# Kernel optimization log

Hardware: AMD Instinct MI355X
Metric: run time of the kernel (lower is better)

The kernel has to match this reference:

```python
import jax, jax.numpy as jnp
import numpy as np

NEG_INF = -1e30  # stands in for -inf on the H-diagonal (matches softmax zeroing)


def conv1x1(x, W, b):
    # x: [B,C,H,W], W: [O,C], b: [O] -> [B,O,H,W]
    return jnp.einsum('bchw,oc->bohw', x, W) + b[None, :, None, None]


def setup_inputs() -> dict:
    key = jax.random.key(0)
    ks = jax.random.split(key, 8)
    B, C, H, W = 4, 64, 256, 256
    C8 = C // 8
    s = 1.0 / np.sqrt(C)
    return {
        'x': jax.random.normal(ks[0], (B, C, H, W), jnp.float32),
        'Wq': jax.random.normal(ks[1], (C8, C), jnp.float32) * s,
        'bq': jnp.zeros((C8,), jnp.float32),
        'Wk': jax.random.normal(ks[2], (C8, C), jnp.float32) * s,
        'bk': jnp.zeros((C8,), jnp.float32),
        'Wv': jax.random.normal(ks[3], (C, C), jnp.float32) * s,
        'bv': jnp.zeros((C,), jnp.float32),
        'gamma': jnp.zeros((1,), jnp.float32),
    }


def reference(x, Wq, bq, Wk, bk, Wv, bv, gamma):
    B, C, H, W = x.shape
    q = conv1x1(x, Wq, bq)   # [B,C8,H,W]
    k = conv1x1(x, Wk, bk)   # [B,C8,H,W]
    v = conv1x1(x, Wv, bv)   # [B,C,H,W]

    # Row (height-axis) attention energies with -inf on the self (diagonal) entry.
    energy_H = jnp.einsum('bchw,bcjw->bhwj', q, k)               # [B,H,W,H]
    diag = jnp.eye(H, dtype=bool)[:, None, :]                    # [H,1,H]
    energy_H = jnp.where(diag[None], NEG_INF, energy_H)
    # Column (width-axis) attention energies.
    energy_W = jnp.einsum('bchw,bchj->bhwj', q, k)               # [B,H,W,W]

    att = jax.nn.softmax(jnp.concatenate([energy_H, energy_W], axis=3), axis=3)
    att_H, att_W = att[..., :H], att[..., H:]                    # [B,H,W,H], [B,H,W,W]

    out_H = jnp.einsum('bcjw,bhwj->bchw', v, att_H)
    out_W = jnp.einsum('bchj,bhwj->bchw', v, att_W)
    return gamma[0] * (out_H + out_W) + x
```

## Files before the change

kernel.cpp:

```cpp
#include <hip/hip_runtime.h>

#define Bn 4
#define Cn 64
#define Hn 256
#define Wn 256
#define HWn 65536

typedef unsigned int u32;
typedef __attribute__((ext_vector_type(2))) unsigned int u32x2;
typedef __attribute__((ext_vector_type(8))) short bf16x8;
typedef __attribute__((ext_vector_type(4))) float f32x4;
typedef __attribute__((ext_vector_type(16))) float f32x16;

__device__ __forceinline__ unsigned short f2b(float f) {
    union { float f; unsigned u; } v; v.f = f;
    return (unsigned short)(v.u >> 16);
}
__device__ __forceinline__ float b2f(unsigned short s) {
    union { float f; unsigned u; } v; v.u = ((unsigned)s) << 16;
    return v.f;
}
__device__ __forceinline__ u32 cvtpk(float lo, float hi) {
    u32 r;
    asm("v_cvt_pk_bf16_f32 %0, %1, %2" : "=v"(r) : "v"(lo), "v"(hi));
    return r;
}
__device__ __forceinline__ void vswap(u32& a, u32& b) {
    asm volatile("v_permlane32_swap_b32 %0, %1" : "+v"(a), "+v"(b));
}
__device__ __forceinline__ float pair_other(float v, int lane) {
    union { float f; u32 u; } A; A.f = v;
    u32 a = A.u, b = A.u;
    vswap(a, b);
    union { u32 u; float f; } R; R.u = (lane < 32) ? b : a;
    return R.f;
}
__device__ __forceinline__ bf16x8 expPack(const f32x16& e, int base, float& ss) {
    float p0 = __expf(e[base + 0]), p1 = __expf(e[base + 1]);
    u32 A = cvtpk(p0, p1); ss += p0 + p1;
    float p4 = __expf(e[base + 4]), p5 = __expf(e[base + 5]);
    u32 B = cvtpk(p4, p5); ss += p4 + p5;
    vswap(A, B);
    float p2 = __expf(e[base + 2]), p3 = __expf(e[base + 3]);
    u32 C = cvtpk(p2, p3); ss += p2 + p3;
    float p6 = __expf(e[base + 6]), p7 = __expf(e[base + 7]);
    u32 D = cvtpk(p6, p7); ss += p6 + p7;
    vswap(C, D);
    union { u32 w[4]; bf16x8 v; } u;
    u.w[0] = A; u.w[1] = C; u.w[2] = B; u.w[3] = D;
    return u.v;
}

__global__ __launch_bounds__(256) void k_proj(
    const float* __restrict__ x,
    const float* __restrict__ Wq, const float* __restrict__ bq,
    const float* __restrict__ Wk, const float* __restrict__ bk,
    const float* __restrict__ Wv, const float* __restrict__ bv,
    unsigned short* __restrict__ qbr, unsigned short* __restrict__ kbr,
    unsigned short* __restrict__ v_row)
{
    __shared__ __align__(16) char Xl[2][16384];
    int t = threadIdx.x, lane = t & 63, wv = t >> 6;
    int row16 = lane & 15, g = lane >> 4;
    int u0 = blockIdx.x * 4;

    bf16x8 Af[5][2];
    #pragma unroll
    for (int m = 0; m < 5; ++m) {
        const float* wrow;
        if (m == 0) wrow = (row16 < 8) ? (Wq + row16 * 64) : (Wk + (row16 - 8) * 64);
        else        wrow = Wv + (size_t)((m - 1) * 16 + row16) * 64;
        #pragma unroll
        for (int ks = 0; ks < 2; ++ks) {
            int c0 = ks * 32 + g * 8;
            f32x4 w0 = *(const f32x4*)(wrow + c0);
            f32x4 w1 = *(const f32x4*)(wrow + c0 + 4);
            bf16x8 a;
            a[0] = (short)f2b(w0[0]); a[1] = (short)f2b(w0[1]);
            a[2] = (short)f2b(w0[2]); a[3] = (short)f2b(w0[3]);
            a[4] = (short)f2b(w1[0]); a[5] = (short)f2b(w1[1]);
            a[6] = (short)f2b(w1[2]); a[7] = (short)f2b(w1[3]);
            Af[m][ks] = a;
        }
    }

    int px4 = (t & 31) * 4;
    int cbase = (t >> 5) << 2;

    f32x4 st[2][8];
    {
        int u = u0;
        int b = u >> 9, rest = u & 511, h = rest >> 1, half = rest & 1;
        const float* xb2 = x + (size_t)b * Cn * HWn + (size_t)h * Wn + half * 128;
        #pragma unroll
        for (int pass = 0; pass < 2; ++pass) {
            int c0s = cbase + pass * 32;
            #pragma unroll
            for (int j = 0; j < 4; ++j)
                st[0][pass * 4 + j] = *(const f32x4*)(xb2 + (size_t)(c0s + j) * HWn + px4);
        }
    }

    #pragma unroll
    for (int ui = 0; ui < 4; ++ui) {
        int u = u0 + ui;
        int b = u >> 9, rest = u & 511, h = rest >> 1, half = rest & 1;
        int cur = ui & 1;

        #pragma unroll
        for (int pass = 0; pass < 2; ++pass) {
            int c0s = cbase + pass * 32;
            #pragma unroll
            for (int i = 0; i < 4; ++i) {
                int px = px4 + i;
                u32x2 w;
                w[0] = (u32)f2b(st[cur][pass * 4 + 0][i]) | ((u32)f2b(st[cur][pass * 4 + 1][i]) << 16);
                w[1] = (u32)f2b(st[cur][pass * 4 + 2][i]) | ((u32)f2b(st[cur][pass * 4 + 3][i]) << 16);
                unsigned addr = (unsigned)(px * 128)
                              + (((unsigned)(c0s * 2)) ^ ((((unsigned)px >> 3) & 7) << 4));
                *(u32x2*)(Xl[cur] + addr) = w;
            }
        }
        __syncthreads();

        if (ui < 3) {
            int un = u + 1;
            int bn = un >> 9, restn = un & 511, hn = restn >> 1, halfn = restn & 1;
            const float* xb2 = x + (size_t)bn * Cn * HWn + (size_t)hn * Wn + halfn * 128;
            #pragma unroll
            for (int pass = 0; pass < 2; ++pass) {
                int c0s = cbase + pass * 32;
                #pragma unroll
                for (int j = 0; j < 4; ++j)
                    st[cur ^ 1][pass * 4 + j] = *(const f32x4*)(xb2 + (size_t)(c0s + j) * HWn + px4);
            }
        }

        f32x4 acc[5][2];
        #pragma unroll
        for (int m = 0; m < 5; ++m)
            #pragma unroll
            for (int nt = 0; nt < 2; ++nt)
                acc[m][nt] = (f32x4){0.f, 0.f, 0.f, 0.f};

        #pragma unroll
        for (int nt = 0; nt < 2; ++nt) {
            int px = wv * 32 + nt * 16 + row16;
            #pragma unroll
            for (int ks = 0; ks < 2; ++ks) {
                int c0 = ks * 32 + g * 8;
                unsigned addr = (unsigned)(px * 128)
                              + (((unsigned)(c0 * 2)) ^ ((((unsigned)px >> 3) & 7) << 4));
                bf16x8 bf = *(const bf16x8*)(Xl[cur] + addr);
                #pragma unroll
                for (int m = 0; m < 5; ++m)
                    acc[m][nt] = __builtin_amdgcn_mfma_f32_16x16x32_bf16(Af[m][ks], bf, acc[m][nt], 0, 0, 0);
            }
        }

        f32x4 bQK = (g < 2) ? *(const f32x4*)(bq + g * 4)
                            : *(const f32x4*)(bk + (g - 2) * 4);
        #pragma unroll
        for (int nt = 0; nt < 2; ++nt) {
            int p = half * 128 + wv * 32 + nt * 16 + row16;
            f32x4 d = acc[0][nt];
            d[0] += bQK[0]; d[1] += bQK[1]; d[2] += bQK[2]; d[3] += bQK[3];
            u32 w0 = (u32)f2b(d[0]) | ((u32)f2b(d[1]) << 16);
            u32 w1 = (u32)f2b(d[2]) | ((u32)f2b(d[3]) << 16);
            size_t roff = ((size_t)(b * Hn + h) * Wn + p) * 8 + (size_t)((g & 1) * 4);
            if (g < 2) {
                *(u32*)(qbr + roff) = w0; *(u32*)(qbr + roff + 2) = w1;
            } else {
                *(u32*)(kbr + roff) = w0; *(u32*)(kbr + roff + 2) = w1;
            }
            #pragma unroll
            for (int m = 1; m < 5; ++m) {
                f32x4 bV = *(const f32x4*)(bv + (m - 1) * 16 + g * 4);
                unsigned short* vp = v_row + (size_t)b * Cn * HWn
                                   + (size_t)((m - 1) * 16 + g * 4) * HWn
                                   + (size_t)h * Wn + p;
                #pragma unroll
                for (int r = 0; r < 4; ++r)
                    vp[(size_t)r * HWn] = f2b(acc[m][nt][r] + bV[r]);
            }
        }
    }
}

__global__ __launch_bounds__(256) void k_tr_bf16(
    const unsigned short* __restrict__ in, unsigned short* __restrict__ out,
    int R, int Ccols)
{
    __shared__ unsigned short tile[64][66];
    int t = threadIdx.x;
    int lr = t >> 6, lc = t & 63;
    int tilesC = Ccols >> 6;
    int per_b = (R >> 6) * tilesC;
    int bid = blockIdx.x;
    int b = bid / per_b;
    int rem = bid - b * per_b;
    int r0 = (rem / tilesC) << 6;
    int c0 = (rem - (rem / tilesC) * tilesC) << 6;
    const unsigned short* ip = in + (size_t)b * R * Ccols;
    unsigned short* op = out + (size_t)b * R * Ccols;
    #pragma unroll
    for (int i = 0; i < 16; ++i) {
        int r = lr * 16 + i;
        tile[r][lc] = ip[(size_t)(r0 + r) * Ccols + c0 + lc];
    }
    __syncthreads();
    #pragma unroll
    for (int i = 0; i < 16; ++i) {
        int c = lr * 16 + i;
        op[(size_t)(c0 + c) * R + r0 + lc] = tile[lc][c];
    }
}

__global__ __launch_bounds__(256, 2) void k_attnH(
    const unsigned short* __restrict__ qbr, const unsigned short* __restrict__ kbr,
    const unsigned short* __restrict__ vT,
    unsigned short* __restrict__ ohT,
    float* __restrict__ sH)
{
    __shared__ __align__(16) unsigned short Vl[16384];
    int t = threadIdx.x, lane = t & 63, wv = t >> 6;
    int l31 = lane & 31, hi = lane >> 5;
    int bid = blockIdx.x;
    int qh = bid & 1;
    int rest = bid >> 1, b = rest >> 8, w = rest & 255;

    const char* vsrc = (const char*)(vT + ((size_t)(b * Wn + w)) * Cn * Hn);
    #pragma unroll
    for (int p = 0; p < 8; ++p) {
        int lin = p * 4096 + t * 16;
        int c = lin >> 9;
        f32x4 d = *(const f32x4*)(vsrc + lin);
        unsigned dst = (unsigned)lin ^ ((unsigned)(c & 7) << 4);
        *(f32x4*)((char*)Vl + dst) = d;
    }

    bf16x8 zer = {};
    int qtA = qh * 4 + wv;
    int q = qtA * 32 + l31;
    bf16x8 Qf, Kf[8];
    {
        bf16x8 v = *(const bf16x8*)(qbr + ((size_t)(b * Hn + q) * Wn + w) * 8);
        Qf = (hi == 0) ? v : zer;
    }
    #pragma unroll
    for (int jt = 0; jt < 8; ++jt) {
        int j = jt * 32 + l31;
        bf16x8 v = *(const bf16x8*)(kbr + ((size_t)(b * Hn + j) * Wn + w) * 8);
        Kf[jt] = (hi == 0) ? v : zer;
    }
    __syncthreads();

    f32x16 Oa = {}, Ob = {};
    float s = 0.f;
    #pragma unroll
    for (int jt = 0; jt < 8; ++jt) {
        f32x16 zc = {};
        f32x16 e = __builtin_amdgcn_mfma_f32_32x32x16_bf16(Kf[jt], Qf, zc, 0, 0, 0);
        if (jt == qtA) {
            #pragma unroll
            for (int r = 0; r < 16; ++r) {
                int rl = (r & 3) + 8 * (r >> 2) + 4 * hi;
                e[r] = (rl == l31) ? -1e30f : e[r];
            }
        }
        bf16x8 P0 = expPack(e, 0, s);
        bf16x8 P1 = expPack(e, 8, s);
        #pragma unroll
        for (int k2 = 0; k2 < 2; ++k2) {
            int ktA = jt * 2 + k2;
            bf16x8 Pf = k2 ? P1 : P0;
            #pragma unroll
            for (int ct = 0; ct < 2; ++ct) {
                int c = ct * 32 + l31;
                unsigned ad = ((unsigned)(c * 512 + ktA * 32 + hi * 16))
                            ^ ((unsigned)(c & 7) << 4);
                bf16x8 Vf = *(const bf16x8*)((const char*)Vl + ad);
                if (ct == 0) Oa = __builtin_amdgcn_mfma_f32_32x32x16_bf16(Vf, Pf, Oa, 0, 0, 0);
                else         Ob = __builtin_amdgcn_mfma_f32_32x32x16_bf16(Vf, Pf, Ob, 0, 0, 0);
            }
        }
    }
    float s_tot = s + pair_other(s, lane);
    if (hi == 0) {
        size_t so = ((size_t)(b * Wn + w)) * Hn + q;
        sH[so] = s_tot;
    }
    unsigned short* ob = ohT + ((size_t)(b * Wn + w)) * Cn * Hn;
    #pragma unroll
    for (int ct = 0; ct < 2; ++ct) {
        #pragma unroll
        for (int r = 0; r < 16; ++r) {
            int c = (r & 3) + 8 * (r >> 2) + 4 * hi + ct * 32;
            float val = ct ? Ob[r] : Oa[r];
            ob[(size_t)c * Hn + q] = f2b(val);
        }
    }
}

__global__ __launch_bounds__(256, 2) void k_attnW(
    const unsigned short* __restrict__ qbr, const unsigned short* __restrict__ kbr,
    const unsigned short* __restrict__ v_row,
    const unsigned short* __restrict__ oh_row,
    const float* __restrict__ sH,
    const float* __restrict__ x, const float* __restrict__ gamma,
    float* __restrict__ out)
{
    __shared__ __align__(16) unsigned short Vl[16384];
    int t = threadIdx.x, lane = t & 63, wv = t >> 6;
    int l31 = lane & 31, hi = lane >> 5;
    int bid = blockIdx.x;
    int qh = bid & 1;
    int rest = bid >> 1, b = rest >> 8, h = rest & 255;

    #pragma unroll
    for (int p = 0; p < 8; ++p) {
        int lin = p * 4096 + t * 16;
        int c = lin >> 9, off = lin & 511;
        const char* src = (const char*)(v_row + ((size_t)(b * Cn + c)) * HWn + (size_t)h * Wn) + off;
        f32x4 d = *(const f32x4*)src;
        unsigned dst = (unsigned)lin ^ ((unsigned)(c & 7) << 4);
        *(f32x4*)((char*)Vl + dst) = d;
    }

    const unsigned short* qb = qbr + ((size_t)(b * Hn + h)) * Wn * 8;
    const unsigned short* kb = kbr + ((size_t)(b * Hn + h)) * Wn * 8;
    bf16x8 zer = {};
    int q = qh * 128 + wv * 32 + l31;
    bf16x8 Qf, Kf[8];
    {
        bf16x8 v = *(const bf16x8*)(qb + (size_t)q * 8);
        Qf = (hi == 0) ? v : zer;
    }
    #pragma unroll
    for (int jt = 0; jt < 8; ++jt) {
        int j = jt * 32 + l31;
        bf16x8 v = *(const bf16x8*)(kb + (size_t)j * 8);
        Kf[jt] = (hi == 0) ? v : zer;
    }
    float g = gamma[0];
    __syncthreads();

    f32x16 Oa = {}, Ob = {};
    float s = 0.f;
    #pragma unroll
    for (int jt = 0; jt < 8; ++jt) {
        f32x16 zc = {};
        f32x16 e = __builtin_amdgcn_mfma_f32_32x32x16_bf16(Kf[jt], Qf, zc, 0, 0, 0);
        bf16x8 P0 = expPack(e, 0, s);
        bf16x8 P1 = expPack(e, 8, s);
        #pragma unroll
        for (int k2 = 0; k2 < 2; ++k2) {
            int ktA = jt * 2 + k2;
            bf16x8 Pf = k2 ? P1 : P0;
            #pragma unroll
            for (int ct = 0; ct < 2; ++ct) {
                int c = ct * 32 + l31;
                unsigned ad = ((unsigned)(c * 512 + ktA * 32 + hi * 16))
                            ^ ((unsigned)(c & 7) << 4);
                bf16x8 Vf = *(const bf16x8*)((const char*)Vl + ad);
                if (ct == 0) Oa = __builtin_amdgcn_mfma_f32_32x32x16_bf16(Vf, Pf, Oa, 0, 0, 0);
                else         Ob = __builtin_amdgcn_mfma_f32_32x32x16_bf16(Vf, Pf, Ob, 0, 0, 0);
            }
        }
    }
    float s_tot = s + pair_other(s, lane);
    size_t so = ((size_t)(b * Wn + q)) * Hn + h;
    float sh = sH[so];
    float gi = g / (s_tot + sh);
    #pragma unroll
    for (int ct = 0; ct < 2; ++ct) {
        #pragma unroll
        for (int r = 0; r < 16; ++r) {
            int c = (r & 3) + 8 * (r >> 2) + 4 * hi + ct * 32;
            size_t idx = ((size_t)(b * Cn + c) * Hn + h) * Wn + q;
            float val = ct ? Ob[r] : Oa[r];
            out[idx] = gi * (val + b2f(oh_row[idx])) + x[idx];
        }
    }
}

extern "C" void kernel_launch(void* const* d_in, const int* in_sizes, int n_in,
                              void* d_out, int out_size, void* d_ws, size_t ws_size,
                              hipStream_t stream) {
    const float* x  = (const float*)d_in[0];
    const float* Wq = (const float*)d_in[1];
    const float* bq = (const float*)d_in[2];
    const float* Wk = (const float*)d_in[3];
    const float* bk = (const float*)d_in[4];
    const float* Wv = (const float*)d_in[5];
    const float* bv = (const float*)d_in[6];
    const float* gm = (const float*)d_in[7];
    float* out = (float*)d_out;
    char* ws = (char*)d_ws;

    const size_t BHW = (size_t)Bn * Hn * Wn;
    unsigned short* qbr = (unsigned short*)ws;
    unsigned short* kbr = qbr + 8 * BHW;
    unsigned short* v_row = kbr + 8 * BHW;
    unsigned short* vT    = v_row + 64 * BHW;
    unsigned short* ohT   = vT + 64 * BHW;
    unsigned short* oh_row = vT;
    float* sHb = (float*)(ohT + 64 * BHW);

    k_proj<<<512, 256, 0, stream>>>(x, Wq, bq, Wk, bk, Wv, bv,
                                    qbr, kbr, v_row);
    k_tr_bf16<<<Bn * (16384 / 64) * (256 / 64), 256, 0, stream>>>(v_row, vT, 16384, 256);
    k_attnH<<<Bn * Wn * 2, 256, 0, stream>>>(qbr, kbr, vT, ohT, sHb);
    k_tr_bf16<<<Bn * (256 / 64) * (16384 / 64), 256, 0, stream>>>(ohT, oh_row, 256, 16384);
    k_attnW<<<Bn * Hn * 2, 256, 0, stream>>>(qbr, kbr, v_row, oh_row, sHb, x, gm, out);
}
```

Measured before the change: 114.4 us.

## Store H-attention output channel-last to drop the intermediate transpose kernel

```diff
diff --git a/kernel.cpp b/kernel.cpp
--- a/kernel.cpp
+++ b/kernel.cpp
@@ -219,7 +219,7 @@
 __global__ __launch_bounds__(256, 2) void k_attnH(
     const unsigned short* __restrict__ qbr, const unsigned short* __restrict__ kbr,
     const unsigned short* __restrict__ vT,
-    unsigned short* __restrict__ ohT,
+    unsigned short* __restrict__ ohp,
     float* __restrict__ sH)
 {
     __shared__ __align__(16) unsigned short Vl[16384];
@@ -290,14 +290,17 @@
         size_t so = ((size_t)(b * Wn + w)) * Hn + q;
         sH[so] = s_tot;
     }
-    unsigned short* ob = ohT + ((size_t)(b * Wn + w)) * Cn * Hn;
+    unsigned short* ob = ohp + (((size_t)(b * Wn + w) * Hn + q) * Cn);
     #pragma unroll
     for (int ct = 0; ct < 2; ++ct) {
         #pragma unroll
-        for (int r = 0; r < 16; ++r) {
-            int c = (r & 3) + 8 * (r >> 2) + 4 * hi + ct * 32;
-            float val = ct ? Ob[r] : Oa[r];
-            ob[(size_t)c * Hn + q] = f2b(val);
+        for (int rq = 0; rq < 4; ++rq) {
+            int c0 = ct * 32 + rq * 8 + 4 * hi;
+            const f32x16& O = ct ? Ob : Oa;
+            u32x2 wv2;
+            wv2[0] = cvtpk(O[rq * 4 + 0], O[rq * 4 + 1]);
+            wv2[1] = cvtpk(O[rq * 4 + 2], O[rq * 4 + 3]);
+            *(u32x2*)(ob + c0) = wv2;
         }
     }
 }
@@ -305,7 +308,7 @@
 __global__ __launch_bounds__(256, 2) void k_attnW(
     const unsigned short* __restrict__ qbr, const unsigned short* __restrict__ kbr,
     const unsigned short* __restrict__ v_row,
-    const unsigned short* __restrict__ oh_row,
+    const unsigned short* __restrict__ ohp,
     const float* __restrict__ sH,
     const float* __restrict__ x, const float* __restrict__ gamma,
     float* __restrict__ out)
@@ -372,14 +375,21 @@
     size_t so = ((size_t)(b * Wn + q)) * Hn + h;
     float sh = sH[so];
     float gi = g / (s_tot + sh);
+    const unsigned short* op = ohp + (((size_t)(b * Wn + q) * Hn + h) * Cn);
     #pragma unroll
     for (int ct = 0; ct < 2; ++ct) {
         #pragma unroll
-        for (int r = 0; r < 16; ++r) {
-            int c = (r & 3) + 8 * (r >> 2) + 4 * hi + ct * 32;
-            size_t idx = ((size_t)(b * Cn + c) * Hn + h) * Wn + q;
-            float val = ct ? Ob[r] : Oa[r];
-            out[idx] = gi * (val + b2f(oh_row[idx])) + x[idx];
+        for (int rq = 0; rq < 4; ++rq) {
+            int c0 = ct * 32 + rq * 8 + 4 * hi;
+            u32x2 wv2 = *(const u32x2*)(op + c0);
+            const f32x16& O = ct ? Ob : Oa;
+            #pragma unroll
+            for (int j = 0; j < 4; ++j) {
+                int c = c0 + j;
+                size_t idx = ((size_t)(b * Cn + c) * Hn + h) * Wn + q;
+                unsigned short oh16 = (unsigned short)((wv2[j >> 1] >> ((j & 1) * 16)) & 0xffff);
+                out[idx] = gi * (O[rq * 4 + j] + b2f(oh16)) + x[idx];
+            }
         }
     }
 }
@@ -403,14 +413,12 @@
     unsigned short* kbr = qbr + 8 * BHW;
     unsigned short* v_row = kbr + 8 * BHW;
     unsigned short* vT    = v_row + 64 * BHW;
-    unsigned short* ohT   = vT + 64 * BHW;
-    unsigned short* oh_row = vT;
-    float* sHb = (float*)(ohT + 64 * BHW);
+    unsigned short* ohp   = vT + 64 * BHW;
+    float* sHb = (float*)(ohp + 64 * BHW);
 
     k_proj<<<512, 256, 0, stream>>>(x, Wq, bq, Wk, bk, Wv, bv,
                                     qbr, kbr, v_row);
     k_tr_bf16<<<Bn * (16384 / 64) * (256 / 64), 256, 0, stream>>>(v_row, vT, 16384, 256);
-    k_attnH<<<Bn * Wn * 2, 256, 0, stream>>>(qbr, kbr, vT, ohT, sHb);
-    k_tr_bf16<<<Bn * (256 / 64) * (16384 / 64), 256, 0, stream>>>(ohT, oh_row, 256, 16384);
-    k_attnW<<<Bn * Hn * 2, 256, 0, stream>>>(qbr, kbr, v_row, oh_row, sHb, x, gm, out);
-}
+    k_attnH<<<Bn * Wn * 2, 256, 0, stream>>>(qbr, kbr, vT, ohp, sHb);
+    k_attnW<<<Bn * Hn * 2, 256, 0, stream>>>(qbr, kbr, v_row, ohp, sHb, x, gm, out);
+}
```

Measured after the change: 108.1 us (median of 2 runs). 5.5% less time.
